# Performance work log

Measured on AMD Instinct MI355X. Metric: run time of the kernel, lower is better.

Reference implementation:

```python
import jax, jax.numpy as jnp
import numpy as np

HEADS = 6


def setup_inputs() -> dict:
    key = jax.random.key(0)
    ks = jax.random.split(key, 4)
    B, N, C = 4, 1024, 384
    s = 0.02
    return {
        "x": jax.random.normal(ks[0], (B, N, C), jnp.float32),
        "qkv_w": jax.random.normal(ks[1], (C, 3 * C), jnp.float32) * s,  # (in, out) layout
        "qkv_b": jnp.zeros((3 * C,), jnp.float32),
        "proj_w": jax.random.normal(ks[2], (C, C), jnp.float32) * s,
        "proj_b": jnp.zeros((C,), jnp.float32),
        "conv_w": jax.random.normal(ks[3], (HEADS, HEADS), jnp.float32) * s,  # 1x1 conv kernel (out_ch, in_ch)
        "conv_b": jnp.zeros((HEADS,), jnp.float32),
    }


def _forward(x, qkv_w, qkv_b, proj_w, proj_b, conv_w, conv_b):
    B, N, C = x.shape
    H = HEADS
    D = C // H
    scale = D ** -0.5
    qkv = (x @ qkv_w + qkv_b).reshape(B, N, 3, H, D)
    q = jnp.transpose(qkv[:, :, 0], (0, 2, 1, 3))  # bhnd
    k = jnp.transpose(qkv[:, :, 1], (0, 2, 1, 3))
    v = jnp.transpose(qkv[:, :, 2], (0, 2, 1, 3))
    qk = jnp.einsum('bhnd,bhmd->bhnm', q, k)          # raw scores (pre-scale)
    attn_mean = jax.nn.softmax(qk * scale, axis=-1)
    # data_uncertainty: 1x1 conv mixing the head channels of qk
    u = jnp.einsum('oh,bhnm->bonm', conv_w, qk) + conv_b[None, :, None, None]
    # norm_uncertainty: log(exp(u)) == u (kept faithful), then (tanh+1)/2
    u = jnp.log(jnp.exp(u))
    u = (jnp.tanh(u) + 1.0) * 0.5
    # gumbel-softmax (hard, tau=1) over logits [u, 1-u]; channel 1 selected.
    # softmax over 2 classes == sigmoid of logit difference; hard == argmax.
    gk = jax.random.key(42)
    g0 = jax.random.gumbel(jax.random.fold_in(gk, 0), u.shape, u.dtype)
    g1 = jax.random.gumbel(jax.random.fold_in(gk, 1), u.shape, u.dtype)
    l0 = u + g0
    l1 = (1.0 - u) + g1
    soft1 = jax.nn.sigmoid(l1 - l0)
    hard1 = (l1 > l0).astype(u.dtype)
    mask = hard1 + soft1 - jax.lax.stop_gradient(soft1)  # straight-through estimator
    attn = attn_mean * mask  # attn_drop is identity in eval / dropout=0
    out = jnp.einsum('bhnm,bhmd->bnhd', attn, v).reshape(B, N, C)
    out = out @ proj_w + proj_b  # proj_drop identity
    return out, attn_mean, u


def reference(x, qkv_w, qkv_b, proj_w, proj_b, conv_w, conv_b):
    return _forward(x, qkv_w, qkv_b, proj_w, proj_b, conv_w, conv_b)
```

## Files before the change

### kernel.cpp

```cpp
#include <hip/hip_runtime.h>
#include <hip/hip_bf16.h>
#include <stdint.h>
#include <stddef.h>

#define B_ 4
#define N_ 1024
#define C_ 384
#define H_ 6
#define D_ 64
#define TC_ 1152
#define BHNN_ 25165824
#define SCALE 0.125f
#define LOG2E 1.4426950408889634f
#define LN2 0.6931471805599453f

typedef __hip_bfloat16 bf16;
typedef __attribute__((ext_vector_type(2))) float f32x2;
typedef __attribute__((ext_vector_type(4))) float f32x4;
typedef __attribute__((ext_vector_type(8))) short short8;

union f4u { f32x4 v4; f32x2 v2[2]; };

__device__ __forceinline__ short f2bs(float x){
  bf16 b = __float2bfloat16(x);
  return *reinterpret_cast<short*>(&b);
}

__device__ __forceinline__ void pk_fma_ll(f32x2& c, f32x2 a, f32x2 b){
  asm("v_pk_fma_f32 %0, %1, %2, %0 op_sel:[0,0,0] op_sel_hi:[0,1,1]" : "+v"(c) : "v"(a), "v"(b));
}
__device__ __forceinline__ void pk_fma_hh(f32x2& c, f32x2 a, f32x2 b){
  asm("v_pk_fma_f32 %0, %1, %2, %0 op_sel:[1,0,0] op_sel_hi:[1,1,1]" : "+v"(c) : "v"(a), "v"(b));
}

#define TFR(x0,x1,r) { x0 += x1; x1 = ((x1)<<(r))|((x1)>>(32-(r))); x1 ^= x0; }

__host__ __device__ __forceinline__ void tf2x32(uint32_t k0, uint32_t k1,
                                                uint32_t& x0, uint32_t& x1){
  uint32_t k2 = k0 ^ k1 ^ 0x1BD11BDAu;
  x0 += k0; x1 += k1;
  TFR(x0,x1,13) TFR(x0,x1,15) TFR(x0,x1,26) TFR(x0,x1,6)
  x0 += k1; x1 += k2 + 1u;
  TFR(x0,x1,17) TFR(x0,x1,29) TFR(x0,x1,16) TFR(x0,x1,24)
  x0 += k2; x1 += k0 + 2u;
  TFR(x0,x1,13) TFR(x0,x1,15) TFR(x0,x1,26) TFR(x0,x1,6)
  x0 += k0; x1 += k1 + 3u;
  TFR(x0,x1,17) TFR(x0,x1,29) TFR(x0,x1,16) TFR(x0,x1,24)
  x0 += k1; x1 += k2 + 4u;
  TFR(x0,x1,13) TFR(x0,x1,15) TFR(x0,x1,26) TFR(x0,x1,6)
  x0 += k2; x1 += k0 + 5u;
}

__device__ __forceinline__ uint32_t rotl32(uint32_t x, uint32_t r){
#if __has_builtin(__builtin_amdgcn_alignbit)
  return __builtin_amdgcn_alignbit(x, x, 32u - r);
#else
  return (x << r) | (x >> (32u - r));
#endif
}

__device__ __forceinline__ void tf_dual(uint32_t j,
    uint32_t ak0, uint32_t ak1, uint32_t ak2,
    uint32_t bk0, uint32_t bk1, uint32_t bk2,
    float& fA, float& fB){
  uint32_t x0 = ak0, x1 = j + ak1;
  uint32_t y0 = bk0, y1 = j + bk1;
  #define DTFR(r) { x0 += x1; y0 += y1;               \
                    x1 = rotl32(x1,(r)); y1 = rotl32(y1,(r)); \
                    x1 ^= x0; y1 ^= y0; }
  DTFR(13) DTFR(15) DTFR(26) DTFR(6)
  x0 += ak1; x1 += ak2 + 1u;  y0 += bk1; y1 += bk2 + 1u;
  DTFR(17) DTFR(29) DTFR(16) DTFR(24)
  x0 += ak2; x1 += ak0 + 2u;  y0 += bk2; y1 += bk0 + 2u;
  DTFR(13) DTFR(15) DTFR(26) DTFR(6)
  x0 += ak0; x1 += ak1 + 3u;  y0 += bk0; y1 += bk1 + 3u;
  DTFR(17) DTFR(29) DTFR(16) DTFR(24)
  x0 += ak1; x1 += ak2 + 4u;  y0 += bk1; y1 += bk2 + 4u;
  DTFR(13) DTFR(15) DTFR(26) DTFR(6)
  x0 += ak2; x1 += ak0 + 5u;  y0 += bk2; y1 += bk0 + 5u;
  #undef DTFR
  uint32_t bitsA = x0 ^ x1;
  uint32_t bitsB = y0 ^ y1;
  fA = fmaxf(__uint_as_float((bitsA >> 9) | 0x3F800000u) - 1.0f, 1.1754943508222875e-38f);
  fB = fmaxf(__uint_as_float((bitsB >> 9) | 0x3F800000u) - 1.0f, 1.1754943508222875e-38f);
}

__global__ __launch_bounds__(256) void k_qkv(const float* __restrict__ x,
                                             const float* __restrict__ w,
                                             const float* __restrict__ bias,
                                             bf16* __restrict__ qb,
                                             bf16* __restrict__ kb,
                                             bf16* __restrict__ vTb){
  __shared__ __align__(16) float As[16][68];
  __shared__ __align__(16) float Bs[16][68];
  const int t  = threadIdx.x;
  const int tx = t & 15, ty = t >> 4;
  const int m0 = blockIdx.x * 64, n0 = blockIdx.y * 64;
  const int am = t >> 2,        ak = (t & 3) * 4;
  const int bn = (t & 15) * 4,  bk = t >> 4;
  f32x2 c[4][2] = {};
  for (int k0 = 0; k0 < C_; k0 += 16){
    f32x4 av = *(const f32x4*)&x[(size_t)(m0+am)*C_ + k0 + ak];
    f32x4 bv = *(const f32x4*)&w[(size_t)(k0+bk)*TC_ + n0 + bn];
    __syncthreads();
    As[ak+0][am] = av[0]; As[ak+1][am] = av[1];
    As[ak+2][am] = av[2]; As[ak+3][am] = av[3];
    *(f32x4*)&Bs[bk][bn] = bv;
    __syncthreads();
    #pragma unroll
    for (int k = 0; k < 16; k++){
      f4u a, b;
      a.v4 = *(const f32x4*)&As[k][ty*4];
      b.v4 = *(const f32x4*)&Bs[k][tx*4];
      pk_fma_ll(c[0][0], a.v2[0], b.v2[0]); pk_fma_ll(c[0][1], a.v2[0], b.v2[1]);
      pk_fma_hh(c[1][0], a.v2[0], b.v2[0]); pk_fma_hh(c[1][1], a.v2[0], b.v2[1]);
      pk_fma_ll(c[2][0], a.v2[1], b.v2[0]); pk_fma_ll(c[2][1], a.v2[1], b.v2[1]);
      pk_fma_hh(c[3][0], a.v2[1], b.v2[0]); pk_fma_hh(c[3][1], a.v2[1], b.v2[1]);
    }
  }
  #pragma unroll
  for (int i = 0; i < 4; i++){
    int mg = m0 + ty*4 + i;
    int bb = mg >> 10, nn = mg & 1023;
    #pragma unroll
    for (int jp = 0; jp < 2; jp++){
      #pragma unroll
      for (int sub = 0; sub < 2; sub++){
        int jg = n0 + tx*4 + jp*2 + sub;
        int t3 = jg / C_;
        int rem = jg - t3*C_;
        int h = rem >> 6, d = rem & 63;
        bf16 val = __float2bfloat16(c[i][jp][sub] + bias[jg]);
        if (t3 == 0)      qb[((size_t)(bb*H_ + h)*N_ + nn)*D_ + d] = val;
        else if (t3 == 1) kb[((size_t)(bb*H_ + h)*N_ + nn)*D_ + d] = val;
        else              vTb[((size_t)(bb*H_ + h)*D_ + d)*N_ + nn] = val;
      }
    }
  }
}

__global__ __launch_bounds__(256) void k_scores(const short* __restrict__ qb,
                                                const short* __restrict__ kb,
                                                float* __restrict__ qk){
  const int gw = blockIdx.x * 4 + (threadIdx.x >> 6);
  const int lane = threadIdx.x & 63;
  const int mt = gw & 63, nt = (gw >> 6) & 63, bh = gw >> 12;
  const int lo = lane & 15, quad = lane >> 4;
  const short* qrow = qb + ((size_t)bh*N_ + nt*16 + lo)*D_ + quad*8;
  const short* krow = kb + ((size_t)bh*N_ + mt*16 + lo)*D_ + quad*8;
  short8 a0 = *(const short8*)qrow;
  short8 b0 = *(const short8*)krow;
  short8 a1 = *(const short8*)(qrow + 32);
  short8 b1 = *(const short8*)(krow + 32);
  f32x4 acc = {0.f, 0.f, 0.f, 0.f};
  acc = __builtin_amdgcn_mfma_f32_16x16x32_bf16(a0, b0, acc, 0, 0, 0);
  acc = __builtin_amdgcn_mfma_f32_16x16x32_bf16(a1, b1, acc, 0, 0, 0);
  float* o = qk + (size_t)bh*N_*N_ + (size_t)(nt*16)*N_ + mt*16;
  #pragma unroll
  for (int r = 0; r < 4; r++)
    o[(size_t)(quad*4 + r)*N_ + lo] = acc[r];
}

__global__ __launch_bounds__(256) void k_fuse(float* __restrict__ attn,
                                              const float* __restrict__ cw,
                                              const float* __restrict__ cb,
                                              float* __restrict__ u_out,
                                              unsigned long long* __restrict__ mbits,
                                              uint32_t g0k0, uint32_t g0k1,
                                              uint32_t g1k0, uint32_t g1k1){
  const int bn = blockIdx.x;
  const int bb = bn >> 10, n = bn & 1023;
  const int t = threadIdx.x, lane = t & 63, wid = t >> 6;
  __shared__ float redm[H_][4], reds[H_][4];

  float qv[H_][4];
  #pragma unroll
  for (int h = 0; h < H_; h++){
    const float* p = attn + (((size_t)(bb*H_ + h) << 10) + n) * N_;
    #pragma unroll
    for (int i = 0; i < 4; i++) qv[h][i] = p[t + 256*i];
  }
  #pragma unroll
  for (int h = 0; h < H_; h++){
    float mx = fmaxf(fmaxf(qv[h][0], qv[h][1]), fmaxf(qv[h][2], qv[h][3]));
    #pragma unroll
    for (int off = 32; off > 0; off >>= 1) mx = fmaxf(mx, __shfl_xor(mx, off));
    if (lane == 0) redm[h][wid] = mx;
  }
  __syncthreads();
  float mxh[H_], sm[H_];
  #pragma unroll
  for (int h = 0; h < H_; h++){
    mxh[h] = fmaxf(fmaxf(redm[h][0], redm[h][1]), fmaxf(redm[h][2], redm[h][3]));
    const float k2 = SCALE * LOG2E;
    float s = 0.f;
    #pragma unroll
    for (int i = 0; i < 4; i++) s += __builtin_amdgcn_exp2f((qv[h][i] - mxh[h]) * k2);
    #pragma unroll
    for (int off = 32; off > 0; off >>= 1) s += __shfl_xor(s, off);
    if (lane == 0) reds[h][wid] = s;
    sm[h] = s;
  }
  __syncthreads();
  float invS[H_];
  #pragma unroll
  for (int h = 0; h < H_; h++){
    float S = reds[h][0] + reds[h][1] + reds[h][2] + reds[h][3];
    invS[h] = __builtin_amdgcn_rcpf(S);
  }
  #pragma unroll
  for (int h = 0; h < H_; h++){
    float* p = attn + (((size_t)(bb*H_ + h) << 10) + n) * N_;
    const float k2 = SCALE * LOG2E;
    #pragma unroll
    for (int i = 0; i < 4; i++)
      p[t + 256*i] = __builtin_amdgcn_exp2f((qv[h][i] - mxh[h]) * k2) * invS[h];
  }
  const uint32_t a2k = g0k0 ^ g0k1 ^ 0x1BD11BDAu;
  const uint32_t b2k = g1k0 ^ g1k1 ^ 0x1BD11BDAu;
  const uint32_t jrow = ((uint32_t)(bb*H_) << 20) | ((uint32_t)n << 10);
  #pragma unroll
  for (int i = 0; i < 4; i++){
    const uint32_t m = (uint32_t)(t + 256*i);
    #pragma unroll
    for (int o = 0; o < H_; o++){
      float up = cb[o];
      #pragma unroll
      for (int h = 0; h < H_; h++) up += cw[o*H_ + h] * qv[h][i];
      float eneg = __builtin_amdgcn_exp2f(-2.0f * LOG2E * up);
      float uu   = __builtin_amdgcn_rcpf(1.0f + eneg);
      float tt   = 2.0f * uu - 1.0f;
      float et   = __builtin_amdgcn_exp2f(tt * LOG2E);
      uint32_t j = jrow + ((uint32_t)o << 20) + m;
      float f0, f1;
      tf_dual(j, g0k0, g0k1, a2k, g1k0, g1k1, b2k, f0, f1);
      float L0 = __builtin_amdgcn_logf(f0);
      float L1 = __builtin_amdgcn_logf(f1);
      int hard = L0 < L1 * et;
      u_out[(size_t)j] = uu;
      unsigned long long bal = __ballot(hard);
      if (lane == 0) mbits[(size_t)j >> 6] = bal;
    }
  }
}

__global__ __launch_bounds__(256) void k_av(const float* __restrict__ attn,
                                            const unsigned long long* __restrict__ mbits,
                                            const short* __restrict__ vTb,
                                            float* __restrict__ tmp){
  const int gw = blockIdx.x * 4 + (threadIdx.x >> 6);
  const int lane = threadIdx.x & 63;
  const int pr = gw & 1, nt = (gw >> 1) & 63, bh = gw >> 7;
  const int bb = bh / H_, h = bh - bb*H_;
  const int lo = lane & 15, quad = lane >> 4;
  const int row = nt*16 + lo;
  const float* arow = attn + ((size_t)bh*N_ + row)*N_ + quad*8;
  const unsigned long long* mrow = mbits + (((size_t)bh*N_ + row)*N_ >> 6);
  const short* vrow0 = vTb + ((size_t)bh*D_ + pr*32 + lo)*N_ + quad*8;
  const short* vrow1 = vrow0 + 16*N_;
  f32x4 acc0 = {0.f, 0.f, 0.f, 0.f};
  f32x4 acc1 = {0.f, 0.f, 0.f, 0.f};
  #pragma unroll
  for (int mb = 0; mb < N_; mb += 128){
    f32x4 av0[4], av1[4];
    unsigned long long wb[4];
    short8 b0[4], b1[4];
    #pragma unroll
    for (int s = 0; s < 4; s++){
      int m0 = mb + s*32;
      av0[s] = *(const f32x4*)(arow + m0);
      av1[s] = *(const f32x4*)(arow + m0 + 4);
      wb[s]  = mrow[(m0 + quad*8) >> 6];
      b0[s]  = *(const short8*)(vrow0 + m0);
      b1[s]  = *(const short8*)(vrow1 + m0);
    }
    #pragma unroll
    for (int s = 0; s < 4; s++){
      int m0 = mb + s*32;
      int base = (m0 + quad*8) & 63;
      float vals[8] = {av0[s][0], av0[s][1], av0[s][2], av0[s][3],
                       av1[s][0], av1[s][1], av1[s][2], av1[s][3]};
      short8 a;
      #pragma unroll
      for (int j = 0; j < 8; j++)
        a[j] = f2bs(((wb[s] >> (base + j)) & 1ull) ? vals[j] : 0.0f);
      acc0 = __builtin_amdgcn_mfma_f32_16x16x32_bf16(a, b0[s], acc0, 0, 0, 0);
      acc1 = __builtin_amdgcn_mfma_f32_16x16x32_bf16(a, b1[s], acc1, 0, 0, 0);
    }
  }
  float* o = tmp + ((size_t)(bb*N_) + nt*16)*C_ + h*D_ + pr*32;
  #pragma unroll
  for (int r = 0; r < 4; r++){
    o[(size_t)(quad*4 + r)*C_ + lo]      = acc0[r];
    o[(size_t)(quad*4 + r)*C_ + 16 + lo] = acc1[r];
  }
}

__global__ __launch_bounds__(256) void k_proj(const float* __restrict__ A,
                                              const float* __restrict__ w,
                                              const float* __restrict__ bias,
                                              float* __restrict__ out){
  __shared__ __align__(16) float As[16][36];
  __shared__ __align__(16) float Bs[16][68];
  const int t = threadIdx.x, tx = t & 15, ty = t >> 4;
  const int m0 = blockIdx.x * 32, n0 = blockIdx.y * 64;
  const int am = t >> 3,        ak = (t & 7) * 2;
  const int bn = (t & 15) * 4,  bk = t >> 4;
  f32x2 c[2][2] = {};
  for (int k0 = 0; k0 < C_; k0 += 16){
    f32x2 av = *(const f32x2*)&A[(size_t)(m0+am)*C_ + k0 + ak];
    f32x4 bv = *(const f32x4*)&w[(size_t)(k0+bk)*C_ + n0 + bn];
    __syncthreads();
    As[ak+0][am] = av[0]; As[ak+1][am] = av[1];
    *(f32x4*)&Bs[bk][bn] = bv;
    __syncthreads();
    #pragma unroll
    for (int k = 0; k < 16; k++){
      f32x2 a2 = *(const f32x2*)&As[k][ty*2];
      f4u b; b.v4 = *(const f32x4*)&Bs[k][tx*4];
      pk_fma_ll(c[0][0], a2, b.v2[0]); pk_fma_ll(c[0][1], a2, b.v2[1]);
      pk_fma_hh(c[1][0], a2, b.v2[0]); pk_fma_hh(c[1][1], a2, b.v2[1]);
    }
  }
  #pragma unroll
  for (int i = 0; i < 2; i++)
    #pragma unroll
    for (int jp = 0; jp < 2; jp++)
      #pragma unroll
      for (int sub = 0; sub < 2; sub++){
        int jg = n0 + tx*4 + jp*2 + sub;
        out[(size_t)(m0+ty*2+i)*C_ + jg] = c[i][jp][sub] + bias[jg];
      }
}

extern "C" void kernel_launch(void* const* d_in, const int* in_sizes, int n_in,
                              void* d_out, int out_size, void* d_ws, size_t ws_size,
                              hipStream_t stream) {
  const float* x      = (const float*)d_in[0];
  const float* qkv_w  = (const float*)d_in[1];
  const float* qkv_b  = (const float*)d_in[2];
  const float* proj_w = (const float*)d_in[3];
  const float* proj_b = (const float*)d_in[4];
  const float* conv_w = (const float*)d_in[5];
  const float* conv_b = (const float*)d_in[6];

  float* out      = (float*)d_out;
  float* attn_out = out + (size_t)B_*N_*C_;
  float* u_out    = attn_out + (size_t)BHNN_;

  char* ws = (char*)d_ws;
  bf16* qb   = (bf16*)ws;
  bf16* kb   = (bf16*)(ws + 3145728);
  bf16* vTb  = (bf16*)(ws + 6291456);
  unsigned long long* mbits = (unsigned long long*)(ws + 9437184);
  float* tmp = (float*)(ws + 12582912);

  uint32_t g0k0, g0k1, g1k0, g1k1;
  { uint32_t a = 0u, b = 0u; tf2x32(0u, 42u, a, b); g0k0 = a; g0k1 = b; }
  { uint32_t a = 0u, b = 1u; tf2x32(0u, 42u, a, b); g1k0 = a; g1k1 = b; }

  dim3 blk(256);
  k_qkv   <<<dim3(64, 18),  blk, 0, stream>>>(x, qkv_w, qkv_b, qb, kb, vTb);
  k_scores<<<dim3(24576),   blk, 0, stream>>>((const short*)qb, (const short*)kb, attn_out);
  k_fuse  <<<dim3(4096),    blk, 0, stream>>>(attn_out, conv_w, conv_b,
                                              u_out, mbits,
                                              g0k0, g0k1, g1k0, g1k1);
  k_av    <<<dim3(768),     blk, 0, stream>>>(attn_out, mbits, (const short*)vTb, tmp);
  k_proj  <<<dim3(128, 6),  blk, 0, stream>>>(tmp, proj_w, proj_b, out);
}
```

Baseline: 475.8 us.

## Run QKV projection on bf16 MFMA with split hi/lo precision

Adds a prep kernel that splits x and a transposed qkv weight into bf16 high and low parts. The QKV GEMM then uses three MFMA products per tile (hi*hi, hi*lo, lo*hi) in place of fp32 packed FMAs, aiming to keep near-fp32 accuracy while using matrix cores. It also drops the manual 4-stage prefetch unroll in k_av for a simple per-step loop. The cost is an extra kernel launch and extra workspace traffic for the split operands.

```diff
diff --git a/kernel.cpp b/kernel.cpp
--- a/kernel.cpp
+++ b/kernel.cpp
@@ -18,6 +18,7 @@
 typedef __attribute__((ext_vector_type(2))) float f32x2;
 typedef __attribute__((ext_vector_type(4))) float f32x4;
 typedef __attribute__((ext_vector_type(8))) short short8;
+typedef __attribute__((ext_vector_type(4))) short short4v;
 
 union f4u { f32x4 v4; f32x2 v2[2]; };
 
@@ -85,56 +86,110 @@
   fB = fmaxf(__uint_as_float((bitsB >> 9) | 0x3F800000u) - 1.0f, 1.1754943508222875e-38f);
 }
 
-__global__ __launch_bounds__(256) void k_qkv(const float* __restrict__ x,
-                                             const float* __restrict__ w,
+__global__ __launch_bounds__(256) void k_prep(const float* __restrict__ x,
+                                              const float* __restrict__ w,
+                                              short* __restrict__ xhi, short* __restrict__ xlo,
+                                              short* __restrict__ wThi, short* __restrict__ wTlo){
+  const int t = threadIdx.x;
+  if (blockIdx.x < 432){
+    const int kt = blockIdx.x % 12, nt = blockIdx.x / 12;
+    __shared__ float T[32][33];
+    const int col = t & 31, row8 = t >> 5;
+    #pragma unroll
+    for (int i = 0; i < 4; i++)
+      T[row8 + i*8][col] = w[(size_t)(kt*32 + row8 + i*8)*TC_ + nt*32 + col];
+    __syncthreads();
+    #pragma unroll
+    for (int i = 0; i < 4; i++){
+      int n = nt*32 + row8 + i*8;
+      int k = kt*32 + col;
+      float v = T[col][row8 + i*8];
+      bf16 hb = __float2bfloat16(v);
+      float hf = __bfloat162float(hb);
+      bf16 lb = __float2bfloat16(v - hf);
+      wThi[(size_t)n*C_ + k] = *(short*)&hb;
+      wTlo[(size_t)n*C_ + k] = *(short*)&lb;
+    }
+  } else {
+    const int b2 = blockIdx.x - 432;
+    size_t base = ((size_t)b2*256 + t) * 4;
+    #pragma unroll
+    for (int it = 0; it < 8; it++){
+      size_t idx = base + (size_t)it * 196608;
+      f32x4 v = *(const f32x4*)&x[idx];
+      short4v hs, ls;
+      #pragma unroll
+      for (int jj = 0; jj < 4; jj++){
+        bf16 hb = __float2bfloat16(v[jj]);
+        float hf = __bfloat162float(hb);
+        bf16 lb = __float2bfloat16(v[jj] - hf);
+        hs[jj] = *(short*)&hb; ls[jj] = *(short*)&lb;
+      }
+      *(short4v*)&xhi[idx] = hs;
+      *(short4v*)&xlo[idx] = ls;
+    }
+  }
+}
+
+__global__ __launch_bounds__(256) void k_qkv(const short* __restrict__ xhi,
+                                             const short* __restrict__ xlo,
+                                             const short* __restrict__ wThi,
+                                             const short* __restrict__ wTlo,
                                              const float* __restrict__ bias,
                                              bf16* __restrict__ qb,
                                              bf16* __restrict__ kb,
                                              bf16* __restrict__ vTb){
-  __shared__ __align__(16) float As[16][68];
-  __shared__ __align__(16) float Bs[16][68];
-  const int t  = threadIdx.x;
-  const int tx = t & 15, ty = t >> 4;
+  __shared__ __align__(16) short sA[2][64][32];
+  __shared__ __align__(16) short sB[2][64][32];
+  const int t = threadIdx.x, lane = t & 63, wv = t >> 6;
+  const int lo = lane & 15, quad = lane >> 4;
   const int m0 = blockIdx.x * 64, n0 = blockIdx.y * 64;
-  const int am = t >> 2,        ak = (t & 3) * 4;
-  const int bn = (t & 15) * 4,  bk = t >> 4;
-  f32x2 c[4][2] = {};
-  for (int k0 = 0; k0 < C_; k0 += 16){
-    f32x4 av = *(const f32x4*)&x[(size_t)(m0+am)*C_ + k0 + ak];
-    f32x4 bv = *(const f32x4*)&w[(size_t)(k0+bk)*TC_ + n0 + bn];
+  const int sr = lane >> 2, skq = lane & 3;
+  const short* srcAh = xhi  + (size_t)(m0 + wv*16 + sr)*C_ + skq*8;
+  const short* srcAl = xlo  + (size_t)(m0 + wv*16 + sr)*C_ + skq*8;
+  const short* srcBh = wThi + (size_t)(n0 + wv*16 + sr)*C_ + skq*8;
+  const short* srcBl = wTlo + (size_t)(n0 + wv*16 + sr)*C_ + skq*8;
+  short* dAh = &sA[0][wv*16 + sr][skq*8];
+  short* dAl = &sA[1][wv*16 + sr][skq*8];
+  short* dBh = &sB[0][wv*16 + sr][skq*8];
+  short* dBl = &sB[1][wv*16 + sr][skq*8];
+
+  f32x4 acc[4] = {{0,0,0,0},{0,0,0,0},{0,0,0,0},{0,0,0,0}};
+  for (int k0 = 0; k0 < C_; k0 += 32){
+    short8 ra = *(const short8*)(srcAh + k0);
+    short8 rb = *(const short8*)(srcAl + k0);
+    short8 rc = *(const short8*)(srcBh + k0);
+    short8 rd = *(const short8*)(srcBl + k0);
     __syncthreads();
-    As[ak+0][am] = av[0]; As[ak+1][am] = av[1];
-    As[ak+2][am] = av[2]; As[ak+3][am] = av[3];
-    *(f32x4*)&Bs[bk][bn] = bv;
+    *(short8*)dAh = ra; *(short8*)dAl = rb;
+    *(short8*)dBh = rc; *(short8*)dBl = rd;
     __syncthreads();
-    #pragma unroll
-    for (int k = 0; k < 16; k++){
-      f4u a, b;
-      a.v4 = *(const f32x4*)&As[k][ty*4];
-      b.v4 = *(const f32x4*)&Bs[k][tx*4];
-      pk_fma_ll(c[0][0], a.v2[0], b.v2[0]); pk_fma_ll(c[0][1], a.v2[0], b.v2[1]);
-      pk_fma_hh(c[1][0], a.v2[0], b.v2[0]); pk_fma_hh(c[1][1], a.v2[0], b.v2[1]);
-      pk_fma_ll(c[2][0], a.v2[1], b.v2[0]); pk_fma_ll(c[2][1], a.v2[1], b.v2[1]);
-      pk_fma_hh(c[3][0], a.v2[1], b.v2[0]); pk_fma_hh(c[3][1], a.v2[1], b.v2[1]);
-    }
-  }
-  #pragma unroll
-  for (int i = 0; i < 4; i++){
-    int mg = m0 + ty*4 + i;
-    int bb = mg >> 10, nn = mg & 1023;
-    #pragma unroll
-    for (int jp = 0; jp < 2; jp++){
-      #pragma unroll
-      for (int sub = 0; sub < 2; sub++){
-        int jg = n0 + tx*4 + jp*2 + sub;
-        int t3 = jg / C_;
-        int rem = jg - t3*C_;
-        int h = rem >> 6, d = rem & 63;
-        bf16 val = __float2bfloat16(c[i][jp][sub] + bias[jg]);
-        if (t3 == 0)      qb[((size_t)(bb*H_ + h)*N_ + nn)*D_ + d] = val;
-        else if (t3 == 1) kb[((size_t)(bb*H_ + h)*N_ + nn)*D_ + d] = val;
-        else              vTb[((size_t)(bb*H_ + h)*D_ + d)*N_ + nn] = val;
-      }
+    short8 ah = *(const short8*)&sA[0][wv*16 + lo][quad*8];
+    short8 al = *(const short8*)&sA[1][wv*16 + lo][quad*8];
+    #pragma unroll
+    for (int j = 0; j < 4; j++){
+      short8 bh = *(const short8*)&sB[0][j*16 + lo][quad*8];
+      short8 bl = *(const short8*)&sB[1][j*16 + lo][quad*8];
+      acc[j] = __builtin_amdgcn_mfma_f32_16x16x32_bf16(ah, bh, acc[j], 0, 0, 0);
+      acc[j] = __builtin_amdgcn_mfma_f32_16x16x32_bf16(ah, bl, acc[j], 0, 0, 0);
+      acc[j] = __builtin_amdgcn_mfma_f32_16x16x32_bf16(al, bh, acc[j], 0, 0, 0);
+    }
+  }
+  #pragma unroll
+  for (int j = 0; j < 4; j++){
+    int ng = n0 + j*16 + lo;
+    int t3 = ng / C_;
+    int rem = ng - t3*C_;
+    int hh = rem >> 6, dd = rem & 63;
+    float bsv = bias[ng];
+    #pragma unroll
+    for (int r = 0; r < 4; r++){
+      int mg = m0 + wv*16 + quad*4 + r;
+      int bb = mg >> 10, nn = mg & 1023;
+      bf16 val = __float2bfloat16(acc[j][r] + bsv);
+      if (t3 == 0)      qb[((size_t)(bb*H_ + hh)*N_ + nn)*D_ + dd] = val;
+      else if (t3 == 1) kb[((size_t)(bb*H_ + hh)*N_ + nn)*D_ + dd] = val;
+      else              vTb[((size_t)(bb*H_ + hh)*D_ + dd)*N_ + nn] = val;
     }
   }
 }
@@ -260,33 +315,20 @@
   const short* vrow1 = vrow0 + 16*N_;
   f32x4 acc0 = {0.f, 0.f, 0.f, 0.f};
   f32x4 acc1 = {0.f, 0.f, 0.f, 0.f};
-  #pragma unroll
-  for (int mb = 0; mb < N_; mb += 128){
-    f32x4 av0[4], av1[4];
-    unsigned long long wb[4];
-    short8 b0[4], b1[4];
-    #pragma unroll
-    for (int s = 0; s < 4; s++){
-      int m0 = mb + s*32;
-      av0[s] = *(const f32x4*)(arow + m0);
-      av1[s] = *(const f32x4*)(arow + m0 + 4);
-      wb[s]  = mrow[(m0 + quad*8) >> 6];
-      b0[s]  = *(const short8*)(vrow0 + m0);
-      b1[s]  = *(const short8*)(vrow1 + m0);
-    }
-    #pragma unroll
-    for (int s = 0; s < 4; s++){
-      int m0 = mb + s*32;
-      int base = (m0 + quad*8) & 63;
-      float vals[8] = {av0[s][0], av0[s][1], av0[s][2], av0[s][3],
-                       av1[s][0], av1[s][1], av1[s][2], av1[s][3]};
-      short8 a;
-      #pragma unroll
-      for (int j = 0; j < 8; j++)
-        a[j] = f2bs(((wb[s] >> (base + j)) & 1ull) ? vals[j] : 0.0f);
-      acc0 = __builtin_amdgcn_mfma_f32_16x16x32_bf16(a, b0[s], acc0, 0, 0, 0);
-      acc1 = __builtin_amdgcn_mfma_f32_16x16x32_bf16(a, b1[s], acc1, 0, 0, 0);
-    }
+  for (int m0 = 0; m0 < N_; m0 += 32){
+    f32x4 av0 = *(const f32x4*)(arow + m0);
+    f32x4 av1 = *(const f32x4*)(arow + m0 + 4);
+    unsigned long long wb = mrow[(m0 + quad*8) >> 6];
+    int base = (m0 + quad*8) & 63;
+    float vals[8] = {av0[0], av0[1], av0[2], av0[3], av1[0], av1[1], av1[2], av1[3]};
+    short8 a;
+    #pragma unroll
+    for (int j = 0; j < 8; j++)
+      a[j] = f2bs(((wb >> (base + j)) & 1ull) ? vals[j] : 0.0f);
+    short8 b0 = *(const short8*)(vrow0 + m0);
+    short8 b1 = *(const short8*)(vrow1 + m0);
+    acc0 = __builtin_amdgcn_mfma_f32_16x16x32_bf16(a, b0, acc0, 0, 0, 0);
+    acc1 = __builtin_amdgcn_mfma_f32_16x16x32_bf16(a, b1, acc1, 0, 0, 0);
   }
   float* o = tmp + ((size_t)(bb*N_) + nt*16)*C_ + h*D_ + pr*32;
   #pragma unroll
@@ -349,18 +391,23 @@
   float* u_out    = attn_out + (size_t)BHNN_;
 
   char* ws = (char*)d_ws;
-  bf16* qb   = (bf16*)ws;
-  bf16* kb   = (bf16*)(ws + 3145728);
-  bf16* vTb  = (bf16*)(ws + 6291456);
+  bf16*  qb    = (bf16*)ws;
+  bf16*  kb    = (bf16*)(ws + 3145728);
+  bf16*  vTb   = (bf16*)(ws + 6291456);
   unsigned long long* mbits = (unsigned long long*)(ws + 9437184);
-  float* tmp = (float*)(ws + 12582912);
+  float* tmp   = (float*)(ws + 12582912);
+  short* xhi   = (short*)(ws + 18874368);
+  short* xlo   = (short*)(ws + 22020096);
+  short* wThi  = (short*)(ws + 25165824);
+  short* wTlo  = (short*)(ws + 26050560);
 
   uint32_t g0k0, g0k1, g1k0, g1k1;
   { uint32_t a = 0u, b = 0u; tf2x32(0u, 42u, a, b); g0k0 = a; g0k1 = b; }
   { uint32_t a = 0u, b = 1u; tf2x32(0u, 42u, a, b); g1k0 = a; g1k1 = b; }
 
   dim3 blk(256);
-  k_qkv   <<<dim3(64, 18),  blk, 0, stream>>>(x, qkv_w, qkv_b, qb, kb, vTb);
+  k_prep  <<<dim3(624),     blk, 0, stream>>>(x, qkv_w, xhi, xlo, wThi, wTlo);
+  k_qkv   <<<dim3(64, 18),  blk, 0, stream>>>(xhi, xlo, wThi, wTlo, qkv_b, qb, kb, vTb);
   k_scores<<<dim3(24576),   blk, 0, stream>>>((const short*)qb, (const short*)kb, attn_out);
   k_fuse  <<<dim3(4096),    blk, 0, stream>>>(attn_out, conv_w, conv_b,
                                               u_out, mbits,
```

After: 450.6 us. -5.3%, faster.
